# Optimization experiments

Measured on AMD Instinct MI355X. Metric: run time of the kernel, lower is better.

The kernel has to match this reference:

```python
import jax, jax.numpy as jnp
import numpy as np

DIM = 1024
HEADS = 16
DHEAD = 64
MAXLEN = 512
B = 8
N = 256   # sequence (x) length
M = 256   # memory (h) length; M + N <= MAXLEN
INNER = HEADS * DHEAD


def setup_inputs() -> dict:
    key = jax.random.key(0)
    ks = jax.random.split(key, 8)
    w = lambda k, shape: jax.random.normal(k, shape, jnp.float32) * 0.02
    return {
        "x": jax.random.normal(ks[0], (B, N, DIM), jnp.float32),
        "h": jax.random.normal(ks[1], (B, M, DIM), jnp.float32),
        "Wqkv": w(ks[2], (DIM, 3 * INNER)),
        "Wkr": w(ks[3], (DIM, INNER)),
        "R": jax.random.normal(ks[4], (2 * MAXLEN, DIM), jnp.float32),
        "u": jax.random.normal(ks[5], (DHEAD,), jnp.float32),
        "v": jax.random.normal(ks[6], (DHEAD,), jnp.float32),
        "Wout": w(ks[7], (INNER, DIM)),
        "max_len": MAXLEN,
    }


def reference(x, h, Wqkv, Wkr, R, u, v, Wout, max_len):
    b, n, dim = x.shape
    m = h.shape[1]
    t = m + n
    scale = DHEAD ** -0.5

    cat = jnp.concatenate([h, x], axis=1)                     # [b, t, dim]
    qkv = cat @ Wqkv                                          # [b, t, 3*inner]
    q, k, val = [s.reshape(b, t, HEADS, DHEAD).transpose(0, 2, 1, 3)
                 for s in jnp.split(qkv, 3, axis=-1)]          # [b, h, t, d]

    # shifts[i, j] = (j - i) mod 2L, sliced as in the torch buffer
    ar = jnp.arange(2 * max_len)
    shifts_full = (ar[None, :] - ar[:, None]) % (2 * max_len)
    shifts = shifts_full[:max_len, :max_len][m:m + n, :t]      # [n, t]

    kr = (R @ Wkr)[shifts]                                    # gather: [n, t, inner]
    kr = kr.reshape(n, t, HEADS, DHEAD).transpose(2, 0, 1, 3)  # [h, n, t, d]

    q = q[:, :, m:]                                           # [b, h, n, d]

    term_a = jnp.einsum('bhnd,bhmd->bhnm', q, k)
    term_b = jnp.einsum('bhnd,hnmd->bhnm', q, kr)
    term_c = jnp.einsum('d,bhmd->bhm', u, k)[:, :, None, :]    # broadcast over n
    term_d = jnp.einsum('d,hnmd->hnm', v, kr)[None]            # broadcast over b
    dots = (term_a + term_b + term_c + term_d) * scale         # [b, h, n, t]

    qi = jnp.arange(n)[:, None]
    jm = jnp.arange(m)[None, :]
    js = jnp.arange(n)[None, :]
    mem_mask = jnp.where(qi > jm, -jnp.inf, 0.0)               # [n, m]
    ar_mask = jnp.where(js > qi, -jnp.inf, 0.0)                # [n, n]
    bias = jnp.concatenate([mem_mask, ar_mask], axis=1)[None, None]  # [1,1,n,t]

    attn = jax.nn.softmax(dots + bias, axis=-1)
    out = jnp.einsum('bhnm,bhmd->bhnd', attn, val)             # [b, h, n, d]
    out = out.transpose(0, 2, 1, 3).reshape(b, n, INNER)
    return out @ Wout
```

## Files before the change

### kernel.cpp

```cpp
#include <hip/hip_runtime.h>
#include <hip/hip_bf16.h>
#include <math.h>

typedef unsigned short u16;
typedef short bf16x8 __attribute__((ext_vector_type(8)));
typedef float f32x4 __attribute__((ext_vector_type(4)));

__device__ __forceinline__ u16 f2b(float f) {
    __hip_bfloat16 h = __float2bfloat16(f);
    return *reinterpret_cast<u16*>(&h);
}
__device__ __forceinline__ float b2f(u16 v) {
    __hip_bfloat16 h;
    *reinterpret_cast<u16*>(&h) = v;
    return __bfloat162float(h);
}

__device__ __forceinline__ void gload_lds16(const void* g, void* l) {
    __builtin_amdgcn_global_load_lds(
        (const __attribute__((address_space(1))) void*)g,
        (__attribute__((address_space(3))) void*)l, 16, 0, 0);
}


struct EpiQKV4 {
    u16 *Q, *Kt, *Vt;
    __device__ void operator()(int rowp, int colp, f32x4 vals) const {
        int b = colp >> 9, pos = colp & 511;
        int sec = rowp >> 10, cc = rowp & 1023;
        int head = cc >> 6, d0 = cc & 63;
        if (sec == 0) {
            if (pos < 256) return;
            ushort4 o;
            o.x = f2b(vals[0] * 0.125f); o.y = f2b(vals[1] * 0.125f);
            o.z = f2b(vals[2] * 0.125f); o.w = f2b(vals[3] * 0.125f);
            *(ushort4*)(Q + (long)((head * 8 + b) * 256 + (pos - 256)) * 64 + d0) = o;
        } else if (sec == 1) {
            ushort4 o;
            o.x = f2b(vals[0]); o.y = f2b(vals[1]);
            o.z = f2b(vals[2]); o.w = f2b(vals[3]);
            *(ushort4*)(Kt + (long)((b * 16 + head) * 512 + pos) * 64 + d0) = o;
        } else {
            #pragma unroll
            for (int r = 0; r < 4; ++r)
                Vt[(long)((b * 16 + head) * 64 + d0 + r) * 512 + pos] = f2b(vals[r]);
        }
    }
};

struct EpiStoreBf {
    u16* C; long ldc; long strideZ;
    __device__ void operator()(int z, int row, int col, float val) const {
        C[(long)z * strideZ + (long)row * ldc + col] = f2b(val);
    }
};


template <typename Epi, bool AF32, bool ROWMAP>
__device__ __forceinline__ void gemm_bt_body(char* smem, int bx, int by, int bz,
                                             const void* __restrict__ Av, int lda, long strideAz,
                                             const u16* __restrict__ B, int ldb, long strideBz,
                                             int K, Epi epi) {
    constexpr int LDT = 56;
    u16* As = (u16*)smem;
    u16* Bs = As + 64 * LDT;
    int n0 = bx * 64, m0 = by * 64, z = bz;
    const u16* Bb = B + (long)z * strideBz + (long)n0 * ldb;
    int tid = threadIdx.x;
    int wave = tid >> 6, lane = tid & 63;
    int wm = wave >> 1, wn = wave & 1;
    int lrow = lane & 15, lquad = lane >> 4;
    int srow = tid >> 2, scol = (tid & 3) * 8;
    f32x4 acc[2][2] = {};
    for (int k0 = 0; k0 < K; k0 += 32) {
        if constexpr (AF32) {
            long arow = m0 + srow;
            if constexpr (ROWMAP) arow = (arow < 256) ? 768 + arow : 0;
            const float* src = (const float*)Av + (long)z * strideAz + arow * lda + k0 + scol;
            float4 f0 = *(const float4*)src;
            float4 f1 = *(const float4*)(src + 4);
            bf16x8 vv;
            vv[0] = (short)f2b(f0.x); vv[1] = (short)f2b(f0.y);
            vv[2] = (short)f2b(f0.z); vv[3] = (short)f2b(f0.w);
            vv[4] = (short)f2b(f1.x); vv[5] = (short)f2b(f1.y);
            vv[6] = (short)f2b(f1.z); vv[7] = (short)f2b(f1.w);
            *(bf16x8*)(As + srow * LDT + scol) = vv;
        } else {
            const u16* Ab = (const u16*)Av + (long)z * strideAz + (long)m0 * lda;
            *(bf16x8*)(As + srow * LDT + scol) = *(const bf16x8*)(Ab + (long)srow * lda + k0 + scol);
        }
        *(bf16x8*)(Bs + srow * LDT + scol) = *(const bf16x8*)(Bb + (long)srow * ldb + k0 + scol);
        __syncthreads();
        bf16x8 af[2], bfr[2];
        #pragma unroll
        for (int mt = 0; mt < 2; ++mt)
            af[mt] = *(const bf16x8*)(As + (wm * 32 + mt * 16 + lrow) * LDT + lquad * 8);
        #pragma unroll
        for (int nt = 0; nt < 2; ++nt)
            bfr[nt] = *(const bf16x8*)(Bs + (wn * 32 + nt * 16 + lrow) * LDT + lquad * 8);
        #pragma unroll
        for (int mt = 0; mt < 2; ++mt)
            #pragma unroll
            for (int nt = 0; nt < 2; ++nt)
                acc[mt][nt] = __builtin_amdgcn_mfma_f32_16x16x32_bf16(af[mt], bfr[nt], acc[mt][nt], 0, 0, 0);
        __syncthreads();
    }
    #pragma unroll
    for (int mt = 0; mt < 2; ++mt)
        #pragma unroll
        for (int nt = 0; nt < 2; ++nt)
            #pragma unroll
            for (int r = 0; r < 4; ++r) {
                int row = m0 + wm * 32 + mt * 16 + lquad * 4 + r;
                int col = n0 + wn * 32 + nt * 16 + lrow;
                epi(z, row, col, acc[mt][nt][r]);
            }
}

__global__ __launch_bounds__(256) void prep_kernel(const float* __restrict__ x,
                                                   const float* __restrict__ h,
                                                   u16* __restrict__ catBF,
                                                   const float* __restrict__ Wqkv, u16* __restrict__ WqkvT,
                                                   const float* __restrict__ Wkr,  u16* __restrict__ WkrT,
                                                   const float* __restrict__ Wout, u16* __restrict__ WoutT,
                                                   u16* __restrict__ vtGuard) {
    __shared__ float tile[64][65];
    int bid = blockIdx.x, tid = threadIdx.x;
    if (bid == 3328) {
        ((unsigned int*)vtGuard)[tid] = 0u;
        return;
    }
    if (bid < 2048) {
        int idx = (bid * 256 + tid) * 8;
        int c = idx & 1023, r = idx >> 10;
        int b = r >> 9, pos = r & 511;
        const float* src = (pos < 256) ? h + ((long)(b * 256 + pos) * 1024 + c)
                                       : x + ((long)(b * 256 + pos - 256) * 1024 + c);
        float4 f0 = *(const float4*)src;
        float4 f1 = *(const float4*)(src + 4);
        bf16x8 vv;
        vv[0] = (short)f2b(f0.x); vv[1] = (short)f2b(f0.y);
        vv[2] = (short)f2b(f0.z); vv[3] = (short)f2b(f0.w);
        vv[4] = (short)f2b(f1.x); vv[5] = (short)f2b(f1.y);
        vv[6] = (short)f2b(f1.z); vv[7] = (short)f2b(f1.w);
        *(bf16x8*)(catBF + idx) = vv;
        return;
    }
    const float* W; u16* WT; int nb, kb; long ldw;
    int w = bid - 2048;
    if (w < 768) {
        W = Wqkv; WT = WqkvT; ldw = 3072;
        nb = (w % 48) * 64; kb = (w / 48) * 64;
    } else if (w < 1024) {
        int w2 = w - 768;
        W = Wkr; WT = WkrT; ldw = 1024;
        nb = (w2 & 15) * 64; kb = (w2 >> 4) * 64;
    } else {
        int w2 = w - 1024;
        W = Wout; WT = WoutT; ldw = 1024;
        nb = (w2 & 15) * 64; kb = (w2 >> 4) * 64;
    }
    {
        int lr = tid >> 4, lc = (tid & 15) * 4;
        #pragma unroll
        for (int i = 0; i < 4; ++i) {
            float4 v = *(const float4*)&W[(long)(kb + lr + i * 16) * ldw + nb + lc];
            tile[lr + i * 16][lc + 0] = v.x; tile[lr + i * 16][lc + 1] = v.y;
            tile[lr + i * 16][lc + 2] = v.z; tile[lr + i * 16][lc + 3] = v.w;
        }
    }
    __syncthreads();
    {
        int wr = tid >> 2, wc = (tid & 3) * 16;
        #pragma unroll
        for (int k = 0; k < 2; ++k) {
            bf16x8 vv;
            #pragma unroll
            for (int e = 0; e < 8; ++e)
                vv[e] = (short)f2b(tile[wc + k * 8 + e][wr]);
            *(bf16x8*)(WT + (long)(nb + wr) * 1024 + kb + wc + k * 8) = vv;
        }
    }
}

__global__ __launch_bounds__(256, 3) void qkv_rwg_kernel(const u16* __restrict__ A, const u16* __restrict__ B,
                                                         EpiQKV4 eq,
                                                         const float* __restrict__ R, const u16* __restrict__ WkrT,
                                                         u16* __restrict__ RWg) {
    __shared__ alignas(16) char smem[49152];
    int bid0 = blockIdx.x;
    if (bid0 >= 640) {
        int bid2 = bid0 - 640;
        gemm_bt_body<EpiStoreBf, true, true>(smem, bid2 & 15, bid2 >> 4, 0,
            (const void*)R, 1024, 0L, WkrT, 1024, 0L, 1024, EpiStoreBf{RWg, 1024, 0});
        return;
    }
    int xcd = bid0 & 7, s = bid0 >> 3;
    int t0i = s >> 3;
    int w = s & 7;
    int m0, n0;
    if (t0i < 8) {
        int nchunk = xcd >> 1;
        int mrow = (xcd & 1) * 8 + t0i;
        m0 = 1024 + mrow * 128;
        n0 = (nchunk * 8 + w) * 128;
    } else {
        int qidx = xcd * 2 + (t0i - 8);
        int nchunk = qidx >> 3, mrow = qidx & 7;
        m0 = mrow * 128;
        int c = nchunk * 8 + w;
        n0 = (c >> 1) * 512 + 256 + (c & 1) * 128;
    }
    int tid = threadIdx.x, wave = tid >> 6, lane = tid & 63;
    int wm = wave >> 1, wn = wave & 1;
    int lrow = lane & 15, lquad = lane >> 4;
    const u16* Ab = A + (long)m0 * 1024;
    const u16* Bb = B + (long)n0 * 1024;
    f32x4 acc[4][4] = {};

    int scperm = (((tid & 3) - ((tid >> 3) & 3)) & 3) * 8;
    int rsl = ((lquad + (lrow >> 1)) & 3) * 8;

    auto stage = [&](int buf, int k0) {
        u16* Asb = (u16*)smem + buf * 8192;
        u16* Bsb = Asb + 4096;
        int col = k0 + scperm;
        #pragma unroll
        for (int i = 0; i < 2; ++i) {
            int rowb = i * 64 + (tid >> 2);
            gload_lds16(Ab + (long)rowb * 1024 + col, Asb + i * 2048 + tid * 8);
            gload_lds16(Bb + (long)rowb * 1024 + col, Bsb + i * 2048 + tid * 8);
        }
    };
    auto compute = [&](int buf) {
        u16* Asb = (u16*)smem + buf * 8192;
        u16* Bsb = Asb + 4096;
        bf16x8 af[4], bfr[4];
        #pragma unroll
        for (int mt = 0; mt < 4; ++mt)
            af[mt] = *(const bf16x8*)(Asb + (wm * 64 + mt * 16 + lrow) * 32 + rsl);
        #pragma unroll
        for (int nt = 0; nt < 4; ++nt)
            bfr[nt] = *(const bf16x8*)(Bsb + (wn * 64 + nt * 16 + lrow) * 32 + rsl);
        #pragma unroll
        for (int mt = 0; mt < 4; ++mt)
            #pragma unroll
            for (int nt = 0; nt < 4; ++nt)
                acc[mt][nt] = __builtin_amdgcn_mfma_f32_16x16x32_bf16(af[mt], bfr[nt], acc[mt][nt], 0, 0, 0);
    };

    stage(0, 0);
    stage(1, 32);
    int cb = 0, sb = 2;
    for (int t = 0; t < 32; ++t) {
        if (t < 31) {
            asm volatile("s_waitcnt vmcnt(4)" ::: "memory");
        } else {
            asm volatile("s_waitcnt vmcnt(0)" ::: "memory");
        }
        __builtin_amdgcn_sched_barrier(0);
        __builtin_amdgcn_s_barrier();
        __builtin_amdgcn_sched_barrier(0);
        compute(cb);
        __builtin_amdgcn_sched_barrier(0);
        if (t < 30) stage(sb, (t + 2) * 32);
        cb = (cb == 2) ? 0 : cb + 1;
        sb = (sb == 2) ? 0 : sb + 1;
    }

    #pragma unroll
    for (int mt = 0; mt < 4; ++mt)
        #pragma unroll
        for (int nt = 0; nt < 4; ++nt) {
            int rowp = m0 + wm * 64 + mt * 16 + lquad * 4;
            int colp = n0 + wn * 64 + nt * 16 + lrow;
            eq(rowp, colp, acc[mt][nt]);
        }
}

__global__ __launch_bounds__(256, 4) void outproj_kernel(const u16* __restrict__ A,
                                                         const u16* __restrict__ B,
                                                         float* __restrict__ out) {
    __shared__ alignas(16) char smem[16384];
    int bid = blockIdx.x;
    int n0 = (bid & 15) * 64, m0 = (bid >> 4) * 64;
    int tid = threadIdx.x, wave = tid >> 6, lane = tid & 63;
    int wm = wave >> 1, wn = wave & 1;
    int lrow = lane & 15, lquad = lane >> 4;
    const u16* Ab = A + (long)m0 * 1024;
    const u16* Bb = B + (long)n0 * 1024;
    f32x4 acc[2][2] = {};

    int scperm = (((tid & 3) - ((tid >> 3) & 3)) & 3) * 8;
    int rsl = ((lquad + (lrow >> 1)) & 3) * 8;

    auto stage = [&](int buf, int k0) {
        u16* Asb = (u16*)smem + buf * 4096;
        u16* Bsb = Asb + 2048;
        int row = tid >> 2, col = k0 + scperm;
        gload_lds16(Ab + (long)row * 1024 + col, Asb + tid * 8);
        gload_lds16(Bb + (long)row * 1024 + col, Bsb + tid * 8);
    };
    auto compute = [&](int buf) {
        u16* Asb = (u16*)smem + buf * 4096;
        u16* Bsb = Asb + 2048;
        bf16x8 af[2], bfr[2];
        #pragma unroll
        for (int mt = 0; mt < 2; ++mt)
            af[mt] = *(const bf16x8*)(Asb + (wm * 32 + mt * 16 + lrow) * 32 + rsl);
        #pragma unroll
        for (int nt = 0; nt < 2; ++nt)
            bfr[nt] = *(const bf16x8*)(Bsb + (wn * 32 + nt * 16 + lrow) * 32 + rsl);
        #pragma unroll
        for (int mt = 0; mt < 2; ++mt)
            #pragma unroll
            for (int nt = 0; nt < 2; ++nt)
                acc[mt][nt] = __builtin_amdgcn_mfma_f32_16x16x32_bf16(af[mt], bfr[nt], acc[mt][nt], 0, 0, 0);
    };

    stage(0, 0);
    stage(1, 32);
    for (int t = 0; t < 31; ++t) {
        asm volatile("s_waitcnt vmcnt(2)" ::: "memory");
        __builtin_amdgcn_sched_barrier(0);
        __builtin_amdgcn_s_barrier();
        __builtin_amdgcn_sched_barrier(0);
        compute(t & 1);
        __builtin_amdgcn_sched_barrier(0);
        __builtin_amdgcn_s_barrier();
        __builtin_amdgcn_sched_barrier(0);
        if (t < 30) stage(t & 1, (t + 2) * 32);
    }
    asm volatile("s_waitcnt vmcnt(0)" ::: "memory");
    __builtin_amdgcn_sched_barrier(0);
    __builtin_amdgcn_s_barrier();
    __builtin_amdgcn_sched_barrier(0);
    compute(1);

    #pragma unroll
    for (int mt = 0; mt < 2; ++mt)
        #pragma unroll
        for (int nt = 0; nt < 2; ++nt)
            #pragma unroll
            for (int r = 0; r < 4; ++r)
                out[(long)(m0 + wm * 32 + mt * 16 + lquad * 4 + r) * 1024
                    + n0 + wn * 32 + nt * 16 + lrow] = acc[mt][nt][r];
}

__global__ __launch_bounds__(256, 4) void attn_kernel(const u16* __restrict__ Qs,
                                                      const u16* __restrict__ Kt,
                                                      const u16* __restrict__ VT,
                                                      const u16* __restrict__ RWg,
                                                      const float* __restrict__ uvec,
                                                      const float* __restrict__ vvec,
                                                      u16* __restrict__ attnOut) {
    constexpr int LDSW = 360;
    __shared__ alignas(16) u16 SQ[32 * LDSW];
    __shared__ float red[2][4][32];
    int id = blockIdx.x;
    int bh = id & 127, it = id >> 7;
    int b = bh >> 4, h = bh & 15;
    int i0 = it * 32;
    int w0 = i0;
    int tid = threadIdx.x, wave = tid >> 6, lane = tid & 63;
    int lrow = lane & 15, lquad = lane >> 4;

    bf16x8 aq[2][2], aqv[2][2];
    #pragma unroll
    for (int iu = 0; iu < 2; ++iu) {
        const u16* qbase = Qs + (long)((h * 8 + b) * 256 + i0 + iu * 16 + lrow) * 64;
        bf16x8 q0 = *(const bf16x8*)(qbase + lquad * 8);
        bf16x8 q1 = *(const bf16x8*)(qbase + 32 + lquad * 8);
        #pragma unroll
        for (int j = 0; j < 8; ++j) {
            float f0 = b2f((u16)q0[j]), f1 = b2f((u16)q1[j]);
            aq[iu][0][j]  = (short)f2b(f0 + 0.125f * uvec[lquad * 8 + j]);
            aq[iu][1][j]  = (short)f2b(f1 + 0.125f * uvec[32 + lquad * 8 + j]);
            aqv[iu][0][j] = (short)f2b(f0 + 0.125f * vvec[lquad * 8 + j]);
            aqv[iu][1][j] = (short)f2b(f1 + 0.125f * vvec[32 + lquad * 8 + j]);
        }
    }

    const u16* rwbase = RWg + (long)(wave * 80) * 1024 + h * 64;
    #pragma unroll
    for (int t = 0; t < 5; ++t) {
        const u16* rp = rwbase + (long)(t * 16 + lrow) * 1024;
        bf16x8 br0 = *(const bf16x8*)(rp + lquad * 8);
        bf16x8 br1 = *(const bf16x8*)(rp + 32 + lquad * 8);
        int sc = wave * 80 + t * 16 + lrow;
        #pragma unroll
        for (int iu = 0; iu < 2; ++iu) {
            f32x4 qa = {0.f, 0.f, 0.f, 0.f};
            qa = __builtin_amdgcn_mfma_f32_16x16x32_bf16(aqv[iu][0], br0, qa, 0, 0, 0);
            qa = __builtin_amdgcn_mfma_f32_16x16x32_bf16(aqv[iu][1], br1, qa, 0, 0, 0);
            #pragma unroll
            for (int r = 0; r < 4; ++r) {
                int rloc = iu * 16 + lquad * 4 + r;
                SQ[rloc * LDSW + sc + rloc] = f2b(qa[r]);
            }
        }
    }

    const u16* kbase = Kt + ((long)bh * 512 + w0 + wave * 80) * 64;
    bf16x8 bk0[5], bk1[5];
    #pragma unroll
    for (int t = 0; t < 5; ++t) {
        const u16* kp = kbase + (long)(t * 16 + lrow) * 64;
        bk0[t] = *(const bf16x8*)(kp + lquad * 8);
        bk1[t] = *(const bf16x8*)(kp + 32 + lquad * 8);
    }
    f32x4 acc[2][5];
    __builtin_amdgcn_s_setprio(1);
    #pragma unroll
    for (int t = 0; t < 5; ++t)
        #pragma unroll
        for (int iu = 0; iu < 2; ++iu) {
            f32x4 a = {0.f, 0.f, 0.f, 0.f};
            a = __builtin_amdgcn_mfma_f32_16x16x32_bf16(aq[iu][0], bk0[t], a, 0, 0, 0);
            a = __builtin_amdgcn_mfma_f32_16x16x32_bf16(aq[iu][1], bk1[t], a, 0, 0, 0);
            acc[iu][t] = a;
        }
    __builtin_amdgcn_s_setprio(0);
    __syncthreads();

    float m4[2][4];
    #pragma unroll
    for (int iu = 0; iu < 2; ++iu)
        #pragma unroll
        for (int r = 0; r < 4; ++r) m4[iu][r] = -1e30f;
    #pragma unroll
    for (int t = 0; t < 5; ++t) {
        int lj = wave * 80 + t * 16 + lrow;
        #pragma unroll
        for (int iu = 0; iu < 2; ++iu)
            #pragma unroll
            for (int r = 0; r < 4; ++r) {
                int rloc = iu * 16 + lquad * 4 + r;
                bool ok = (unsigned)(lj - rloc) <= 256u;
                float val = ok ? acc[iu][t][r] + b2f(SQ[rloc * LDSW + lj]) : -1e30f;
                acc[iu][t][r] = val;
                m4[iu][r] = fmaxf(m4[iu][r], val);
            }
    }
    #pragma unroll
    for (int iu = 0; iu < 2; ++iu)
        #pragma unroll
        for (int r = 0; r < 4; ++r) {
            #pragma unroll
            for (int off = 1; off < 16; off <<= 1)
                m4[iu][r] = fmaxf(m4[iu][r], __shfl_xor(m4[iu][r], off));
            if (lrow == 0) red[0][wave][iu * 16 + lquad * 4 + r] = m4[iu][r];
        }
    __syncthreads();

    float gmax[2][4];
    #pragma unroll
    for (int iu = 0; iu < 2; ++iu)
        #pragma unroll
        for (int r = 0; r < 4; ++r) {
            int row = iu * 16 + lquad * 4 + r;
            gmax[iu][r] = fmaxf(fmaxf(red[0][0][row], red[0][1][row]),
                                fmaxf(red[0][2][row], red[0][3][row]));
        }

    float s4[2][4] = {};
    #pragma unroll
    for (int t = 0; t < 5; ++t) {
        int lj = wave * 80 + t * 16 + lrow;
        #pragma unroll
        for (int iu = 0; iu < 2; ++iu)
            #pragma unroll
            for (int r = 0; r < 4; ++r) {
                float p = __expf(acc[iu][t][r] - gmax[iu][r]);
                s4[iu][r] += p;
                SQ[(iu * 16 + lquad * 4 + r) * LDSW + lj] = f2b(p);
            }
    }
    #pragma unroll
    for (int iu = 0; iu < 2; ++iu)
        #pragma unroll
        for (int r = 0; r < 4; ++r) {
            #pragma unroll
            for (int off = 1; off < 16; off <<= 1)
                s4[iu][r] += __shfl_xor(s4[iu][r], off);
            if (lrow == 0) red[1][wave][iu * 16 + lquad * 4 + r] = s4[iu][r];
        }
    __syncthreads();

    const u16* vbase = VT + ((long)bh * 64 + wave * 16 + lrow) * 512 + w0;
    f32x4 oacc[2] = {};
    bf16x8 vp[10];
    #pragma unroll
    for (int t = 0; t < 10; ++t)
        vp[t] = *(const bf16x8*)(vbase + t * 32 + lquad * 8);
    __builtin_amdgcn_s_setprio(1);
    #pragma unroll
    for (int t = 0; t < 10; ++t)
        #pragma unroll
        for (int iu = 0; iu < 2; ++iu) {
            bf16x8 ap = *(const bf16x8*)(SQ + (iu * 16 + lrow) * LDSW + t * 32 + lquad * 8);
            oacc[iu] = __builtin_amdgcn_mfma_f32_16x16x32_bf16(ap, vp[t], oacc[iu], 0, 0, 0);
        }
    __builtin_amdgcn_s_setprio(0);
    #pragma unroll
    for (int iu = 0; iu < 2; ++iu)
        #pragma unroll
        for (int r = 0; r < 4; ++r) {
            int row = iu * 16 + lquad * 4 + r;
            float inv = 1.0f / (red[1][0][row] + red[1][1][row] + red[1][2][row] + red[1][3][row]);
            attnOut[(long)(b * 256 + i0 + row) * 1024 + h * 64 + wave * 16 + lrow] = f2b(oacc[iu][r] * inv);
        }
}


extern "C" void kernel_launch(void* const* d_in, const int* in_sizes, int n_in,
                              void* d_out, int out_size, void* d_ws, size_t ws_size,
                              hipStream_t stream) {
    (void)in_sizes; (void)n_in; (void)out_size; (void)ws_size;
    const float* x    = (const float*)d_in[0];
    const float* h    = (const float*)d_in[1];
    const float* Wqkv = (const float*)d_in[2];
    const float* Wkr  = (const float*)d_in[3];
    const float* R    = (const float*)d_in[4];
    const float* u    = (const float*)d_in[5];
    const float* v    = (const float*)d_in[6];
    const float* Wout = (const float*)d_in[7];
    float* out = (float*)d_out;

    char* ws = (char*)d_ws;
    size_t off = 0;
    auto alloc = [&](size_t bytes) -> void* {
        void* p = ws + off;
        off = (off + bytes + 255) & ~(size_t)255;
        return p;
    };
    u16* catBF  = (u16*)alloc(4096L * 1024 * 2);
    u16* WqkvT  = (u16*)alloc(3072L * 1024 * 2);
    u16* WkrT   = (u16*)alloc(1024L * 1024 * 2);
    u16* WoutT  = (u16*)alloc(1024L * 1024 * 2);
    u16* RWg    = (u16*)alloc(320L * 1024 * 2);
    u16* Q      = (u16*)alloc(16L * 8 * 256 * 64 * 2);
    u16* Kt     = (u16*)alloc(8L * 16 * 512 * 64 * 2);
    u16* VT     = (u16*)alloc(8L * 16 * 64 * 512 * 2 + 1024);
    u16* attnO  = (u16*)alloc(2048L * 1024 * 2);
    u16* vtGuard = VT + 8L * 16 * 64 * 512;

    prep_kernel<<<3329, 256, 0, stream>>>(x, h, catBF, Wqkv, WqkvT, Wkr, WkrT, Wout, WoutT, vtGuard);
    qkv_rwg_kernel<<<720, 256, 0, stream>>>(WqkvT, catBF, EpiQKV4{Q, Kt, VT}, R, WkrT, RWg);
    attn_kernel<<<1024, 256, 0, stream>>>(Q, Kt, VT, RWg, u, v, attnO);
    outproj_kernel<<<512, 256, 0, stream>>>(attnO, WoutT, out);
}
```

Before: 161.2 us.

## Route R@Wkr through pipelined 128x128 GEMM path and add XCD-aware attention mapping

The R rows needed for the relative-position GEMM (padded to 384) are now converted to bf16 in the prep kernel. The R@Wkr product then runs through the main pipelined 128x128-tile GEMM loop instead of a separate simple 64x64 GEMM body that converted fp32 inside its loop. This cuts the RWg blocks from 80 to 24 and gives them the same LDS pipelining as the QKV GEMM, at the cost of an extra bf16 buffer and some padded rows. The attention kernel's block index is also remapped so that each XCD handles a contiguous group of batch-heads, aiming for better L2 locality.

```diff
diff --git a/kernel.cpp b/kernel.cpp
--- a/kernel.cpp
+++ b/kernel.cpp
@@ -48,86 +48,33 @@
     }
 };
 
-struct EpiStoreBf {
-    u16* C; long ldc; long strideZ;
-    __device__ void operator()(int z, int row, int col, float val) const {
-        C[(long)z * strideZ + (long)row * ldc + col] = f2b(val);
-    }
-};
-
-
-template <typename Epi, bool AF32, bool ROWMAP>
-__device__ __forceinline__ void gemm_bt_body(char* smem, int bx, int by, int bz,
-                                             const void* __restrict__ Av, int lda, long strideAz,
-                                             const u16* __restrict__ B, int ldb, long strideBz,
-                                             int K, Epi epi) {
-    constexpr int LDT = 56;
-    u16* As = (u16*)smem;
-    u16* Bs = As + 64 * LDT;
-    int n0 = bx * 64, m0 = by * 64, z = bz;
-    const u16* Bb = B + (long)z * strideBz + (long)n0 * ldb;
-    int tid = threadIdx.x;
-    int wave = tid >> 6, lane = tid & 63;
-    int wm = wave >> 1, wn = wave & 1;
-    int lrow = lane & 15, lquad = lane >> 4;
-    int srow = tid >> 2, scol = (tid & 3) * 8;
-    f32x4 acc[2][2] = {};
-    for (int k0 = 0; k0 < K; k0 += 32) {
-        if constexpr (AF32) {
-            long arow = m0 + srow;
-            if constexpr (ROWMAP) arow = (arow < 256) ? 768 + arow : 0;
-            const float* src = (const float*)Av + (long)z * strideAz + arow * lda + k0 + scol;
-            float4 f0 = *(const float4*)src;
-            float4 f1 = *(const float4*)(src + 4);
-            bf16x8 vv;
-            vv[0] = (short)f2b(f0.x); vv[1] = (short)f2b(f0.y);
-            vv[2] = (short)f2b(f0.z); vv[3] = (short)f2b(f0.w);
-            vv[4] = (short)f2b(f1.x); vv[5] = (short)f2b(f1.y);
-            vv[6] = (short)f2b(f1.z); vv[7] = (short)f2b(f1.w);
-            *(bf16x8*)(As + srow * LDT + scol) = vv;
-        } else {
-            const u16* Ab = (const u16*)Av + (long)z * strideAz + (long)m0 * lda;
-            *(bf16x8*)(As + srow * LDT + scol) = *(const bf16x8*)(Ab + (long)srow * lda + k0 + scol);
-        }
-        *(bf16x8*)(Bs + srow * LDT + scol) = *(const bf16x8*)(Bb + (long)srow * ldb + k0 + scol);
-        __syncthreads();
-        bf16x8 af[2], bfr[2];
-        #pragma unroll
-        for (int mt = 0; mt < 2; ++mt)
-            af[mt] = *(const bf16x8*)(As + (wm * 32 + mt * 16 + lrow) * LDT + lquad * 8);
-        #pragma unroll
-        for (int nt = 0; nt < 2; ++nt)
-            bfr[nt] = *(const bf16x8*)(Bs + (wn * 32 + nt * 16 + lrow) * LDT + lquad * 8);
-        #pragma unroll
-        for (int mt = 0; mt < 2; ++mt)
-            #pragma unroll
-            for (int nt = 0; nt < 2; ++nt)
-                acc[mt][nt] = __builtin_amdgcn_mfma_f32_16x16x32_bf16(af[mt], bfr[nt], acc[mt][nt], 0, 0, 0);
-        __syncthreads();
-    }
-    #pragma unroll
-    for (int mt = 0; mt < 2; ++mt)
-        #pragma unroll
-        for (int nt = 0; nt < 2; ++nt)
-            #pragma unroll
-            for (int r = 0; r < 4; ++r) {
-                int row = m0 + wm * 32 + mt * 16 + lquad * 4 + r;
-                int col = n0 + wn * 32 + nt * 16 + lrow;
-                epi(z, row, col, acc[mt][nt][r]);
-            }
-}
-
 __global__ __launch_bounds__(256) void prep_kernel(const float* __restrict__ x,
                                                    const float* __restrict__ h,
                                                    u16* __restrict__ catBF,
                                                    const float* __restrict__ Wqkv, u16* __restrict__ WqkvT,
                                                    const float* __restrict__ Wkr,  u16* __restrict__ WkrT,
                                                    const float* __restrict__ Wout, u16* __restrict__ WoutT,
+                                                   const float* __restrict__ R,   u16* __restrict__ Rg,
                                                    u16* __restrict__ vtGuard) {
     __shared__ float tile[64][65];
     int bid = blockIdx.x, tid = threadIdx.x;
-    if (bid == 3328) {
+    if (bid == 3520) {
         ((unsigned int*)vtGuard)[tid] = 0u;
+        return;
+    }
+    if (bid >= 3328) {
+        int idx = ((bid - 3328) * 256 + tid) * 8;
+        int row = idx >> 10, c = idx & 1023;
+        int srow = (row < 256) ? 768 + row : 0;
+        const float* src = R + (long)srow * 1024 + c;
+        float4 f0 = *(const float4*)src;
+        float4 f1 = *(const float4*)(src + 4);
+        bf16x8 vv;
+        vv[0] = (short)f2b(f0.x); vv[1] = (short)f2b(f0.y);
+        vv[2] = (short)f2b(f0.z); vv[3] = (short)f2b(f0.w);
+        vv[4] = (short)f2b(f1.x); vv[5] = (short)f2b(f1.y);
+        vv[6] = (short)f2b(f1.z); vv[7] = (short)f2b(f1.w);
+        *(bf16x8*)(Rg + idx) = vv;
         return;
     }
     if (bid < 2048) {
@@ -185,37 +132,41 @@
 
 __global__ __launch_bounds__(256, 3) void qkv_rwg_kernel(const u16* __restrict__ A, const u16* __restrict__ B,
                                                          EpiQKV4 eq,
-                                                         const float* __restrict__ R, const u16* __restrict__ WkrT,
+                                                         const u16* __restrict__ Rg, const u16* __restrict__ WkrT,
                                                          u16* __restrict__ RWg) {
     __shared__ alignas(16) char smem[49152];
     int bid0 = blockIdx.x;
-    if (bid0 >= 640) {
-        int bid2 = bid0 - 640;
-        gemm_bt_body<EpiStoreBf, true, true>(smem, bid2 & 15, bid2 >> 4, 0,
-            (const void*)R, 1024, 0L, WkrT, 1024, 0L, 1024, EpiStoreBf{RWg, 1024, 0});
-        return;
-    }
-    int xcd = bid0 & 7, s = bid0 >> 3;
-    int t0i = s >> 3;
-    int w = s & 7;
+    bool isRW = bid0 >= 640;
     int m0, n0;
-    if (t0i < 8) {
-        int nchunk = xcd >> 1;
-        int mrow = (xcd & 1) * 8 + t0i;
-        m0 = 1024 + mrow * 128;
-        n0 = (nchunk * 8 + w) * 128;
+    const u16 *Ag, *Bg;
+    if (isRW) {
+        int b2 = bid0 - 640;
+        m0 = (b2 >> 3) * 128;
+        n0 = (b2 & 7) * 128;
+        Ag = Rg; Bg = WkrT;
     } else {
-        int qidx = xcd * 2 + (t0i - 8);
-        int nchunk = qidx >> 3, mrow = qidx & 7;
-        m0 = mrow * 128;
-        int c = nchunk * 8 + w;
-        n0 = (c >> 1) * 512 + 256 + (c & 1) * 128;
+        int xcd = bid0 & 7, s = bid0 >> 3;
+        int t0i = s >> 3;
+        int w = s & 7;
+        if (t0i < 8) {
+            int nchunk = xcd >> 1;
+            int mrow = (xcd & 1) * 8 + t0i;
+            m0 = 1024 + mrow * 128;
+            n0 = (nchunk * 8 + w) * 128;
+        } else {
+            int qidx = xcd * 2 + (t0i - 8);
+            int nchunk = qidx >> 3, mrow = qidx & 7;
+            m0 = mrow * 128;
+            int c = nchunk * 8 + w;
+            n0 = (c >> 1) * 512 + 256 + (c & 1) * 128;
+        }
+        Ag = A; Bg = B;
     }
     int tid = threadIdx.x, wave = tid >> 6, lane = tid & 63;
     int wm = wave >> 1, wn = wave & 1;
     int lrow = lane & 15, lquad = lane >> 4;
-    const u16* Ab = A + (long)m0 * 1024;
-    const u16* Bb = B + (long)n0 * 1024;
+    const u16* Ab = Ag + (long)m0 * 1024;
+    const u16* Bb = Bg + (long)n0 * 1024;
     f32x4 acc[4][4] = {};
 
     int scperm = (((tid & 3) - ((tid >> 3) & 3)) & 3) * 8;
@@ -268,14 +219,27 @@
         sb = (sb == 2) ? 0 : sb + 1;
     }
 
-    #pragma unroll
-    for (int mt = 0; mt < 4; ++mt)
-        #pragma unroll
-        for (int nt = 0; nt < 4; ++nt) {
-            int rowp = m0 + wm * 64 + mt * 16 + lquad * 4;
-            int colp = n0 + wn * 64 + nt * 16 + lrow;
-            eq(rowp, colp, acc[mt][nt]);
-        }
+    if (isRW) {
+        #pragma unroll
+        for (int mt = 0; mt < 4; ++mt)
+            #pragma unroll
+            for (int nt = 0; nt < 4; ++nt) {
+                int rowp = m0 + wm * 64 + mt * 16 + lquad * 4;
+                int colp = n0 + wn * 64 + nt * 16 + lrow;
+                #pragma unroll
+                for (int r = 0; r < 4; ++r)
+                    RWg[(long)(rowp + r) * 1024 + colp] = f2b(acc[mt][nt][r]);
+            }
+    } else {
+        #pragma unroll
+        for (int mt = 0; mt < 4; ++mt)
+            #pragma unroll
+            for (int nt = 0; nt < 4; ++nt) {
+                int rowp = m0 + wm * 64 + mt * 16 + lquad * 4;
+                int colp = n0 + wn * 64 + nt * 16 + lrow;
+                eq(rowp, colp, acc[mt][nt]);
+            }
+    }
 }
 
 __global__ __launch_bounds__(256, 4) void outproj_kernel(const u16* __restrict__ A,
@@ -357,8 +321,9 @@
     constexpr int LDSW = 360;
     __shared__ alignas(16) u16 SQ[32 * LDSW];
     __shared__ float red[2][4][32];
-    int id = blockIdx.x;
-    int bh = id & 127, it = id >> 7;
+    int xcd = blockIdx.x & 7, local = blockIdx.x >> 3;
+    int bh = xcd * 16 + (local & 15);
+    int it = local >> 4;
     int b = bh >> 4, h = bh & 15;
     int i0 = it * 32;
     int w0 = i0;
@@ -538,15 +503,16 @@
     u16* WqkvT  = (u16*)alloc(3072L * 1024 * 2);
     u16* WkrT   = (u16*)alloc(1024L * 1024 * 2);
     u16* WoutT  = (u16*)alloc(1024L * 1024 * 2);
-    u16* RWg    = (u16*)alloc(320L * 1024 * 2);
+    u16* Rg     = (u16*)alloc(384L * 1024 * 2);
+    u16* RWg    = (u16*)alloc(384L * 1024 * 2);
     u16* Q      = (u16*)alloc(16L * 8 * 256 * 64 * 2);
     u16* Kt     = (u16*)alloc(8L * 16 * 512 * 64 * 2);
     u16* VT     = (u16*)alloc(8L * 16 * 64 * 512 * 2 + 1024);
     u16* attnO  = (u16*)alloc(2048L * 1024 * 2);
     u16* vtGuard = VT + 8L * 16 * 64 * 512;
 
-    prep_kernel<<<3329, 256, 0, stream>>>(x, h, catBF, Wqkv, WqkvT, Wkr, WkrT, Wout, WoutT, vtGuard);
-    qkv_rwg_kernel<<<720, 256, 0, stream>>>(WqkvT, catBF, EpiQKV4{Q, Kt, VT}, R, WkrT, RWg);
+    prep_kernel<<<3521, 256, 0, stream>>>(x, h, catBF, Wqkv, WqkvT, Wkr, WkrT, Wout, WoutT, R, Rg, vtGuard);
+    qkv_rwg_kernel<<<664, 256, 0, stream>>>(WqkvT, catBF, EpiQKV4{Q, Kt, VT}, Rg, WkrT, RWg);
     attn_kernel<<<1024, 256, 0, stream>>>(Q, Kt, VT, RWg, u, v, attnO);
     outproj_kernel<<<512, 256, 0, stream>>>(attnO, WoutT, out);
 }
```

After: 159.9 us. Within noise of the previous version (-0.8%).
